# Kernel optimization log

Hardware: AMD Instinct MI355X
Metric: run time of the kernel (lower is better)

Reference implementation:

```python
import jax, jax.numpy as jnp
import numpy as np

CHUNK_SIZE = 64  # matches init_kwargs chunk_size


def setup_inputs() -> dict:
    key = jax.random.key(0)
    g = jax.random.normal(key, (16, 16384, 64), dtype=jnp.float32)  # [B, T, H]
    return {"g": g}


def reference(g) -> jnp.ndarray:
    # Chunk-local cumsum along T: each chunk of CHUNK_SIZE has an independent
    # inclusive prefix sum (no carry across chunks), matching the torch loop.
    B, T, H = g.shape
    n_chunks = T // CHUNK_SIZE  # T chosen as multiple of CHUNK_SIZE
    gc = g.reshape(B, n_chunks, CHUNK_SIZE, H)
    out = jnp.cumsum(gc, axis=2).reshape(B, T, H).astype(jnp.float32)
    return out
```

## Files before the change

### kernel.cpp

```cpp
#include <hip/hip_runtime.h>


__global__ __launch_bounds__(256, 4) void chunk_cumsum_kernel(
    const float4* __restrict__ g, float4* __restrict__ out) {
    const int tid = blockIdx.x * blockDim.x + threadIdx.x;
    const int h4  = tid & 15;
    const int q   = (tid >> 4) & 3;
    const long col = tid >> 6;

    const long base = col * 1024 + (long)q * 256 + h4;
    const float4* gp = g + base;
    float4*       op = out + base;

    float4 v[16];
#pragma unroll
    for (int t = 0; t < 16; ++t) v[t] = gp[(long)t * 16];

#pragma unroll
    for (int t = 1; t < 16; ++t) {
        v[t].x += v[t - 1].x; v[t].y += v[t - 1].y;
        v[t].z += v[t - 1].z; v[t].w += v[t - 1].w;
    }

    float4 tot = v[15];
    float4 c;  c.x = 0.f; c.y = 0.f; c.z = 0.f; c.w = 0.f;

    float4 u1;
    u1.x = __shfl_up(tot.x, 16, 64);
    u1.y = __shfl_up(tot.y, 16, 64);
    u1.z = __shfl_up(tot.z, 16, 64);
    u1.w = __shfl_up(tot.w, 16, 64);
    float4 p = tot;
    if (q >= 1) {
        c.x += u1.x; c.y += u1.y; c.z += u1.z; c.w += u1.w;
        p.x += u1.x; p.y += u1.y; p.z += u1.z; p.w += u1.w;
    }
    float4 u2;
    u2.x = __shfl_up(p.x, 32, 64);
    u2.y = __shfl_up(p.y, 32, 64);
    u2.z = __shfl_up(p.z, 32, 64);
    u2.w = __shfl_up(p.w, 32, 64);
    if (q >= 2) {
        c.x += u2.x; c.y += u2.y; c.z += u2.z; c.w += u2.w;
    }

#pragma unroll
    for (int t = 0; t < 16; ++t) {
        float4 r;
        r.x = v[t].x + c.x; r.y = v[t].y + c.y;
        r.z = v[t].z + c.z; r.w = v[t].w + c.w;
        op[(long)t * 16] = r;
    }
}

extern "C" void kernel_launch(void* const* d_in, const int* in_sizes, int n_in,
                              void* d_out, int out_size, void* d_ws, size_t ws_size,
                              hipStream_t stream) {
    const float4* g   = (const float4*)d_in[0];
    float4*       out = (float4*)d_out;
    const int threads = 256;
    const int blocks  = 262144 / threads;
    chunk_cumsum_kernel<<<blocks, threads, 0, stream>>>(g, out);
}
```

Measured before the change: 26.10 us.

## Split each chunk across two wavefronts with LDS carry exchange

Each 64-row chunk is now handled by 128 threads (two wavefronts) instead of 64, with each thread loading 8 float4 instead of 16. The first half's chunk total is passed to the second half through shared memory behind a block barrier, and the grid doubles. This aims to raise occupancy and memory-level parallelism for a bandwidth-bound kernel. In exchange it adds a __syncthreads and an LDS round trip, and each thread keeps fewer loads in flight.

```diff
diff --git a/kernel.cpp b/kernel.cpp
--- a/kernel.cpp
+++ b/kernel.cpp
@@ -1,29 +1,31 @@
 #include <hip/hip_runtime.h>
 
 
-__global__ __launch_bounds__(256, 4) void chunk_cumsum_kernel(
+__global__ __launch_bounds__(256, 8) void chunk_cumsum_kernel(
     const float4* __restrict__ g, float4* __restrict__ out) {
-    const int tid = blockIdx.x * blockDim.x + threadIdx.x;
-    const int h4  = tid & 15;
-    const int q   = (tid >> 4) & 3;
-    const long col = tid >> 6;
+    const int tid  = blockIdx.x * blockDim.x + threadIdx.x;
+    const int lane = threadIdx.x & 63;
+    const int h4   = lane & 15;
+    const int s    = lane >> 4;
+    const int half = (tid >> 6) & 1;
+    const long col = tid >> 7;
 
-    const long base = col * 1024 + (long)q * 256 + h4;
+    const long base = col * 1024 + (long)half * 512 + (long)s * 128 + h4;
     const float4* gp = g + base;
     float4*       op = out + base;
 
-    float4 v[16];
+    float4 v[8];
 #pragma unroll
-    for (int t = 0; t < 16; ++t) v[t] = gp[(long)t * 16];
+    for (int k = 0; k < 8; ++k) v[k] = gp[(long)k * 16];
 
 #pragma unroll
-    for (int t = 1; t < 16; ++t) {
-        v[t].x += v[t - 1].x; v[t].y += v[t - 1].y;
-        v[t].z += v[t - 1].z; v[t].w += v[t - 1].w;
+    for (int k = 1; k < 8; ++k) {
+        v[k].x += v[k - 1].x; v[k].y += v[k - 1].y;
+        v[k].z += v[k - 1].z; v[k].w += v[k - 1].w;
     }
 
-    float4 tot = v[15];
-    float4 c;  c.x = 0.f; c.y = 0.f; c.z = 0.f; c.w = 0.f;
+    float4 tot = v[7];
+    float4 c; c.x = 0.f; c.y = 0.f; c.z = 0.f; c.w = 0.f;
 
     float4 u1;
     u1.x = __shfl_up(tot.x, 16, 64);
@@ -31,7 +33,7 @@
     u1.z = __shfl_up(tot.z, 16, 64);
     u1.w = __shfl_up(tot.w, 16, 64);
     float4 p = tot;
-    if (q >= 1) {
+    if (s >= 1) {
         c.x += u1.x; c.y += u1.y; c.z += u1.z; c.w += u1.w;
         p.x += u1.x; p.y += u1.y; p.z += u1.z; p.w += u1.w;
     }
@@ -40,16 +42,30 @@
     u2.y = __shfl_up(p.y, 32, 64);
     u2.z = __shfl_up(p.z, 32, 64);
     u2.w = __shfl_up(p.w, 32, 64);
-    if (q >= 2) {
+    if (s >= 2) {
         c.x += u2.x; c.y += u2.y; c.z += u2.z; c.w += u2.w;
     }
 
+    __shared__ float4 lds_tot[2][16];
+    const int cb = threadIdx.x >> 7;
+    if (half == 0 && s == 3) {
+        float4 ht;
+        ht.x = c.x + tot.x; ht.y = c.y + tot.y;
+        ht.z = c.z + tot.z; ht.w = c.w + tot.w;
+        lds_tot[cb][h4] = ht;
+    }
+    __syncthreads();
+    if (half == 1) {
+        float4 h0 = lds_tot[cb][h4];
+        c.x += h0.x; c.y += h0.y; c.z += h0.z; c.w += h0.w;
+    }
+
 #pragma unroll
-    for (int t = 0; t < 16; ++t) {
+    for (int k = 0; k < 8; ++k) {
         float4 r;
-        r.x = v[t].x + c.x; r.y = v[t].y + c.y;
-        r.z = v[t].z + c.z; r.w = v[t].w + c.w;
-        op[(long)t * 16] = r;
+        r.x = v[k].x + c.x; r.y = v[k].y + c.y;
+        r.z = v[k].z + c.z; r.w = v[k].w + c.w;
+        op[(long)k * 16] = r;
     }
 }
 
@@ -59,6 +75,6 @@
     const float4* g   = (const float4*)d_in[0];
     float4*       out = (float4*)d_out;
     const int threads = 256;
-    const int blocks  = 262144 / threads;
+    const int blocks  = 524288 / threads;
     chunk_cumsum_kernel<<<blocks, threads, 0, stream>>>(g, out);
 }
```

Result: faster. 25.47 us (-2.4%).
